# Kernel tuning notes

Hardware: AMD Instinct MI355X
Metric: run time of the kernel (lower is better)

The kernel has to match this reference:

```python
import jax, jax.numpy as jnp
import numpy as np

B, S, D, H, R = 2, 2048, 1024, 16, 64
DD = D // H  # head depth = 64
EPS = 1e-06


def setup_inputs() -> dict:
    key = jax.random.key(0)
    ks = jax.random.split(key, 12)
    sc = 1.0 / np.sqrt(D)
    inp = {
        'v': jax.random.normal(ks[0], (B, S, D), jnp.float32),
        'k': jax.random.normal(ks[1], (B, S, D), jnp.float32),
        'q': jax.random.normal(ks[2], (B, S, D), jnp.float32),
        'wq_w': jax.random.normal(ks[3], (D, D), jnp.float32) * sc,
        'wq_b': jnp.zeros((D,), jnp.float32),
        'wk_w': jax.random.normal(ks[4], (D, D), jnp.float32) * sc,
        'wk_b': jnp.zeros((D,), jnp.float32),
        'wv_w': jax.random.normal(ks[5], (D, D), jnp.float32) * sc,
        'wv_b': jnp.zeros((D,), jnp.float32),
        'wc_w': jax.random.normal(ks[6], (D, D), jnp.float32) * sc,
        'wc_b': jnp.zeros((D,), jnp.float32),
        # random-feature projection (orthogonal in original; gaussian suffices for a math-equivalent reference)
        'wg': jax.random.normal(ks[7], (H, DD, R), jnp.float32) * (1.0 / np.sqrt(DD)),
    }
    return inp


def _split_heads(x):
    # [B,S,D] -> [B,H,S,DD]
    return x.reshape(B, S, H, DD).transpose(0, 2, 1, 3)


def _combine_heads(x):
    # [B,H,S,DD] -> [B,S,D]
    return x.transpose(0, 2, 1, 3).reshape(B, S, D)


def _sm_approx(x, wg):
    # x: [B,H,S,DD], wg: [H,DD,R] -> phi(x): [B,H,S,R]
    rsqr_d = 1.0 / np.sqrt(DD)
    h_x = jnp.exp(-0.5 * jnp.sum(jnp.square(x), axis=-1, keepdims=True))
    phi_x = rsqr_d * jnp.exp(jnp.einsum('bhsd,hdr->bhsr', x, wg))
    return h_x * phi_x


def reference(v, k, q, wq_w, wq_b, wk_w, wk_b, wv_w, wv_b, wc_w, wc_b, wg):
    norm_d = float(DD) ** -0.25
    qh = _split_heads((q @ wq_w + wq_b) * norm_d)   # [B,H,S,DD]
    kh = _split_heads((k @ wk_w + wk_b) * norm_d)   # [B,H,S,DD]
    vh = _split_heads(v @ wv_w + wv_b)              # [B,H,S,DD]

    q_prime = _sm_approx(qh, wg)                    # [B,H,S,R]
    k_prime = _sm_approx(kh, wg)                    # [B,H,S,R]

    # per-position outer product k_prime (x) v : [B,H,S,R,DD]
    kv_prime = jnp.einsum('bhsr,bhsd->bhsrd', k_prime, vh)

    # causal prefix sums over sequence axis (k_prev/kv_prev = 0 case)
    k_prefix = jnp.cumsum(k_prime, axis=2)          # [B,H,S,R]
    kv_prefix = jnp.cumsum(kv_prime, axis=2)        # [B,H,S,R,DD]

    qk_prefix = jnp.sum(q_prime * k_prefix, axis=-1, keepdims=True)       # [B,H,S,1]
    attn_unnorm = jnp.einsum('bhsr,bhsrd->bhsd', q_prime, kv_prefix)      # [B,H,S,DD]
    attn = attn_unnorm / (EPS + qk_prefix)

    out = _combine_heads(attn) @ wc_w + wc_b        # [B,S,D]
    return (k_prefix, kv_prefix, out)
```

## Files before the change

kernel.cpp:

```cpp
#include <hip/hip_runtime.h>
#include <hip/hip_bf16.h>

#define BB 2
#define SS 2048
#define DD 1024
#define HH 16
#define RR 64
#define DH 64
#define BH (BB*HH)
#define MM (BB*SS)
#define CH 32
#define NCH (SS/CH)
#define CSROW (RR*DH + RR)

using short8 = __attribute__((ext_vector_type(8))) short;
using f32x4  = __attribute__((ext_vector_type(4))) float;

typedef const __attribute__((address_space(1))) unsigned int* gp_t;
typedef __attribute__((address_space(3))) unsigned int* lp_t;

__device__ __forceinline__ void gll16(const void* g, void* l) {
    __builtin_amdgcn_global_load_lds((gp_t)g, (lp_t)l, 16, 0, 0);
}

__device__ __forceinline__ unsigned short f2bf(float x) {
    __hip_bfloat16 h = __float2bfloat16(x);
    return *(unsigned short*)&h;
}

__global__ __launch_bounds__(256) void k_pre(
    const float* __restrict__ q, const float* __restrict__ k, const float* __restrict__ v,
    const float* __restrict__ bq, const float* __restrict__ bk, const float* __restrict__ bv,
    const float* __restrict__ wq, const float* __restrict__ wk,
    const float* __restrict__ wv, const float* __restrict__ wc,
    const float* __restrict__ wg,
    __hip_bfloat16* __restrict__ Xb, float* __restrict__ biasb,
    __hip_bfloat16* __restrict__ WT, __hip_bfloat16* __restrict__ wcT,
    short* __restrict__ wgbT)
{
    int bid = blockIdx.x;
    __shared__ float tile[64][65];
    if (bid < 12288) {
        int z = bid >> 12;
        int bx = bid & 4095;
        const float* src = (z == 0) ? q : (z == 1) ? k : v;
        size_t i = ((size_t)bx * 256 + threadIdx.x) * 4;
        float4 f = *(const float4*)(src + i);
        __hip_bfloat16* dst = Xb + (size_t)z * 4194304 + i;
        dst[0] = __float2bfloat16(f.x);
        dst[1] = __float2bfloat16(f.y);
        dst[2] = __float2bfloat16(f.z);
        dst[3] = __float2bfloat16(f.w);
        if (bx == 0) {
            const float* bb = (z == 0) ? bq : (z == 1) ? bk : bv;
            for (int t = threadIdx.x; t < 1024; t += 256)
                biasb[z * 1024 + t] = bb[t];
        }
    } else if (bid < 13312) {
        int sub = bid - 12288;
        int zz = sub >> 8;
        sub &= 255;
        const float* W = (zz == 0) ? wq : (zz == 1) ? wk : (zz == 2) ? wv : wc;
        __hip_bfloat16* T = (zz < 3) ? (WT + (size_t)zz * 1048576) : wcT;
        int k0 = (sub >> 4) * 64, n0 = (sub & 15) * 64;
        for (int i = threadIdx.x; i < 4096; i += 256) {
            int r = i >> 6, cc = i & 63;
            tile[r][cc] = W[(size_t)(k0 + r) * 1024 + n0 + cc];
        }
        __syncthreads();
        for (int i = threadIdx.x; i < 4096; i += 256) {
            int nl = i >> 6, kl = i & 63;
            T[(size_t)(n0 + nl) * 1024 + k0 + kl] = __float2bfloat16(tile[kl][nl]);
        }
    } else {
        int hx = bid - 13312;
        for (int i = threadIdx.x; i < 4096; i += 256)
            tile[i >> 6][i & 63] = wg[(size_t)hx * 4096 + i];
        __syncthreads();
        for (int i = threadIdx.x; i < 4096; i += 256) {
            int r = i >> 6, d = i & 63;
            wgbT[(size_t)hx * 4096 + r * 64 + d] = (short)f2bf(tile[d][r]);
        }
    }
}

__global__ __launch_bounds__(256) void gemm_bt(
    const __hip_bfloat16* __restrict__ X, const __hip_bfloat16* __restrict__ WT,
    const float* __restrict__ bias, float* __restrict__ Cout,
    const short* __restrict__ wgbT,
    float* __restrict__ qp_out, float* __restrict__ kp_out2,
    long zsX, long zsW, long zsB, long zsC, int mode)
{
    const int K = 1024, N = 1024;
    int z = blockIdx.z;
    const short* Xz = (const short*)(X + (size_t)z * zsX);
    const short* Wz = (const short*)(WT + (size_t)z * zsW);
    const float* bz = bias + (size_t)z * zsB;
    float* Cz = Cout + (size_t)z * zsC;

    int bid = blockIdx.y * gridDim.x + blockIdx.x;
    int nb_cnt = gridDim.x * gridDim.y;
    int cpx = nb_cnt >> 3;
    int swz = (bid & 7) * cpx + (bid >> 3);
    int nb = swz % gridDim.x;
    int mb = swz / gridDim.x;
    int m0 = mb * 128;
    int n0 = nb * 128;

    __shared__ short smem[18432];
    short* As = smem;
    short* Bs = smem + 4096;
    short* wgT = smem;
    short* xw  = smem + 9216;

    int tid = threadIdx.x;
    int lane = tid & 63;
    int w = tid >> 6;
    int wm = (w >> 1) * 64, wn = (w & 1) * 64;

    f32x4 acc[4][4] = {};

    int srow = tid >> 2;
    int scol = (tid & 3) * 8;
    const short* Ag = Xz + (size_t)(m0 + srow) * K + scol;
    const short* Bg = Wz + (size_t)(n0 + srow) * K + scol;
    short* lA0 = As + tid * 8;
    short* lA1 = As + 64 * 32 + tid * 8;
    short* lB0 = Bs + tid * 8;
    short* lB1 = Bs + 64 * 32 + tid * 8;

    int fr = lane & 15, kg = (lane >> 4) * 8;

    for (int kt = 0; kt < K / 32; ++kt) {
        __syncthreads();
        gll16(Ag + kt * 32, lA0);
        gll16(Ag + (size_t)64 * K + kt * 32, lA1);
        gll16(Bg + kt * 32, lB0);
        gll16(Bg + (size_t)64 * K + kt * 32, lB1);
        __syncthreads();

        short8 af[4], bf[4];
#pragma unroll
        for (int mi = 0; mi < 4; ++mi)
            af[mi] = *(const short8*)&As[(wm + mi * 16 + fr) * 32 + kg];
#pragma unroll
        for (int ni = 0; ni < 4; ++ni)
            bf[ni] = *(const short8*)&Bs[(wn + ni * 16 + fr) * 32 + kg];
#pragma unroll
        for (int mi = 0; mi < 4; ++mi)
#pragma unroll
            for (int ni = 0; ni < 4; ++ni)
                acc[mi][ni] = __builtin_amdgcn_mfma_f32_16x16x32_bf16(af[mi], bf[ni], acc[mi][ni], 0, 0, 0);
    }

    int g = lane >> 4, c4 = lane & 15;

    if (mode == 1 && z < 2) {
        const float nd = 0.35355339059327373f;
        float* O = (z == 0) ? qp_out : kp_out2;
        int h = nb * 2 + (w & 1);
        int b = m0 >> 11;
        float bias_n[4];
#pragma unroll
        for (int ni = 0; ni < 4; ++ni) bias_n[ni] = bz[n0 + wn + ni * 16 + c4];

        __syncthreads();
        {
            int row = tid >> 2, part = tid & 3;
#pragma unroll
            for (int hl = 0; hl < 2; ++hl) {
                const short* src = wgbT + ((size_t)(nb * 2 + hl)) * 4096 + row * 64 + part * 16;
                short8 v0 = *(const short8*)src;
                short8 v1 = *(const short8*)(src + 8);
                *(short8*)&wgT[hl * 4608 + row * 72 + part * 16] = v0;
                *(short8*)&wgT[hl * 4608 + row * 72 + part * 16 + 8] = v1;
            }
        }
        __syncthreads();

        short* xww = xw + w * 2304;
        const short* wgh = wgT + (w & 1) * 4608;

#pragma unroll
        for (int pass = 0; pass < 2; ++pass) {
            float nrm[2][4];
#pragma unroll
            for (int mi_l = 0; mi_l < 2; ++mi_l) {
                int mi = pass * 2 + mi_l;
                float part_n[4] = {0.f, 0.f, 0.f, 0.f};
#pragma unroll
                for (int ni = 0; ni < 4; ++ni)
#pragma unroll
                    for (int i = 0; i < 4; ++i) {
                        float xv = (acc[mi][ni][i] + bias_n[ni]) * nd;
                        part_n[i] += xv * xv;
                        xww[(mi_l * 16 + g * 4 + i) * 72 + ni * 16 + c4] = (short)f2bf(xv);
                    }
#pragma unroll
                for (int i = 0; i < 4; ++i) {
                    float t = part_n[i];
                    t += __shfl_xor(t, 1, 64);
                    t += __shfl_xor(t, 2, 64);
                    t += __shfl_xor(t, 4, 64);
                    t += __shfl_xor(t, 8, 64);
                    nrm[mi_l][i] = t;
                }
            }
            short8 afr[2][2], bfr[4][2];
#pragma unroll
            for (int mi_l = 0; mi_l < 2; ++mi_l)
#pragma unroll
                for (int kk = 0; kk < 2; ++kk)
                    afr[mi_l][kk] = *(const short8*)&xww[(mi_l * 16 + c4) * 72 + kk * 32 + g * 8];
#pragma unroll
            for (int ri = 0; ri < 4; ++ri)
#pragma unroll
                for (int kk = 0; kk < 2; ++kk)
                    bfr[ri][kk] = *(const short8*)&wgh[(ri * 16 + c4) * 72 + kk * 32 + g * 8];
            f32x4 p[2][4] = {};
#pragma unroll
            for (int mi_l = 0; mi_l < 2; ++mi_l)
#pragma unroll
                for (int ri = 0; ri < 4; ++ri)
#pragma unroll
                    for (int kk = 0; kk < 2; ++kk)
                        p[mi_l][ri] = __builtin_amdgcn_mfma_f32_16x16x32_bf16(afr[mi_l][kk], bfr[ri][kk], p[mi_l][ri], 0, 0, 0);
#pragma unroll
            for (int mi_l = 0; mi_l < 2; ++mi_l)
#pragma unroll
                for (int ri = 0; ri < 4; ++ri)
#pragma unroll
                    for (int i = 0; i < 4; ++i) {
                        int mi = pass * 2 + mi_l;
                        float val = 0.125f * __expf(p[mi_l][ri][i] - 0.5f * nrm[mi_l][i]);
                        int row = m0 + wm + mi * 16 + g * 4 + i;
                        int s = row & 2047;
                        O[((size_t)(b * 16 + h) * SS + s) * RR + ri * 16 + c4] = val;
                    }
        }
        return;
    }

    int rg = g * 4;
#pragma unroll
    for (int mi = 0; mi < 4; ++mi)
#pragma unroll
        for (int ni = 0; ni < 4; ++ni) {
            int gn = n0 + wn + ni * 16 + fr;
            float bval = bz[gn];
#pragma unroll
            for (int i = 0; i < 4; ++i) {
                int gm = m0 + wm + mi * 16 + rg + i;
                Cz[(size_t)gm * N + gn] = acc[mi][ni][i] + bval;
            }
        }
}

__global__ __launch_bounds__(64) void k_chunksum(
    const float* __restrict__ kprime, const float* __restrict__ vh,
    float* __restrict__ cs)
{
    int c = blockIdx.x;
    int bh = blockIdx.y;
    int b = bh >> 4, h = bh & 15;
    int lane = threadIdx.x;
    __shared__ float kp[CH][RR];
    __shared__ float vv[CH][RR];
    size_t rowbase = (size_t)bh * SS + c * CH;
    const float* vbase = vh + ((size_t)b * SS + c * CH) * DD + h * DH;
#pragma unroll
    for (int i = 0; i < 8; ++i) {
        int flat = i * 64 + lane;
        int row = flat >> 4, q4 = flat & 15;
        *(f32x4*)&kp[row][q4 * 4] = *(const f32x4*)&kprime[(rowbase + row) * RR + q4 * 4];
        *(f32x4*)&vv[row][q4 * 4] = *(const f32x4*)&vbase[(size_t)row * DD + q4 * 4];
    }
    __syncthreads();

    float st[RR];
#pragma unroll
    for (int r = 0; r < RR; ++r) st[r] = 0.f;
    float kpsum = 0.f;
    for (int s = 0; s < CH; ++s) {
        float vd = vv[s][lane];
        kpsum += kp[s][lane];
#pragma unroll
        for (int rq = 0; rq < RR / 4; ++rq) {
            f32x4 kq = *(const f32x4*)&kp[s][rq * 4];
            st[rq * 4 + 0] += kq[0] * vd;
            st[rq * 4 + 1] += kq[1] * vd;
            st[rq * 4 + 2] += kq[2] * vd;
            st[rq * 4 + 3] += kq[3] * vd;
        }
    }
    float* out = cs + (size_t)(bh * NCH + c) * CSROW;
#pragma unroll
    for (int r = 0; r < RR; ++r) out[r * 64 + lane] = st[r];
    out[4096 + lane] = kpsum;
}

__global__ __launch_bounds__(256) void k_scan(float* __restrict__ cs)
{
    int t = blockIdx.x * 256 + threadIdx.x;
    if (t >= BH * CSROW) return;
    int bh = t / CSROW;
    int e = t - bh * CSROW;
    float* p = cs + (size_t)bh * NCH * CSROW + e;
    float v[NCH];
#pragma unroll
    for (int c = 0; c < NCH; ++c) v[c] = p[(size_t)c * CSROW];
    float run = 0.f;
#pragma unroll
    for (int c = 0; c < NCH; ++c) {
        float x = v[c];
        p[(size_t)c * CSROW] = run;
        run += x;
    }
}

__global__ __launch_bounds__(64) void k_scanfinal(
    const float* __restrict__ kprime, const float* __restrict__ qprime,
    const float* __restrict__ vh, const float* __restrict__ cs,
    float* __restrict__ kp_out, float* __restrict__ kv_out,
    __hip_bfloat16* __restrict__ attnb)
{
    int c = blockIdx.x;
    int bh = blockIdx.y;
    int b = bh >> 4, h = bh & 15;
    int lane = threadIdx.x;
    int g = lane >> 4, c4 = lane & 15;
    __shared__ float kp[CH][RR];
    __shared__ float qp[CH][RR];
    __shared__ float vv[CH][RR];
    size_t rowbase = (size_t)bh * SS + c * CH;
    const float* vbase = vh + ((size_t)b * SS + c * CH) * DD + h * DH;
#pragma unroll
    for (int i = 0; i < 8; ++i) {
        int flat = i * 64 + lane;
        int row = flat >> 4, q4 = flat & 15;
        *(f32x4*)&kp[row][q4 * 4] = *(const f32x4*)&kprime[(rowbase + row) * RR + q4 * 4];
        *(f32x4*)&qp[row][q4 * 4] = *(const f32x4*)&qprime[(rowbase + row) * RR + q4 * 4];
        *(f32x4*)&vv[row][q4 * 4] = *(const f32x4*)&vbase[(size_t)row * DD + q4 * 4];
    }

    const float* off = cs + (size_t)(bh * NCH + c) * CSROW;
    f32x4 st[16];
#pragma unroll
    for (int j = 0; j < 16; ++j)
        st[j] = *(const f32x4*)&off[(4 * j + g) * 64 + 4 * c4];
    float kps = off[4096 + lane];
    __syncthreads();

    for (int s = 0; s < CH; ++s) {
        float kpl = kp[s][lane];
        kps += kpl;
        size_t srow = rowbase + s;
        kp_out[srow * RR + lane] = kps;

        float qksum = qp[s][lane] * kps;
#pragma unroll
        for (int m = 1; m < 64; m <<= 1) qksum += __shfl_xor(qksum, m, 64);

        f32x4 v4 = *(const f32x4*)&vv[s][4 * c4];
        f32x4 accp = {0.f, 0.f, 0.f, 0.f};
        float* kvp = kv_out + srow * (size_t)(RR * DH);
#pragma unroll
        for (int j = 0; j < 16; ++j) {
            float kpj = kp[s][4 * j + g];
            float qpj = qp[s][4 * j + g];
            st[j] += kpj * v4;
            __builtin_nontemporal_store(st[j], (f32x4*)(kvp + (4 * j + g) * 64 + 4 * c4));
            accp += qpj * st[j];
        }
#pragma unroll
        for (int e = 0; e < 4; ++e) {
            accp[e] += __shfl_xor(accp[e], 16, 64);
            accp[e] += __shfl_xor(accp[e], 32, 64);
        }
        float rs = 1.0f / (1e-6f + qksum);
        if (g == 0) {
            ushort4 pkt;
            pkt.x = f2bf(accp[0] * rs);
            pkt.y = f2bf(accp[1] * rs);
            pkt.z = f2bf(accp[2] * rs);
            pkt.w = f2bf(accp[3] * rs);
            *(ushort4*)((unsigned short*)attnb + ((size_t)b * SS + c * CH + s) * DD + h * DH + 4 * c4) = pkt;
        }
    }
}

extern "C" void kernel_launch(void* const* d_in, const int* in_sizes, int n_in,
                              void* d_out, int out_size, void* d_ws, size_t ws_size,
                              hipStream_t stream) {
    const float* v_in  = (const float*)d_in[0];
    const float* k_in  = (const float*)d_in[1];
    const float* q_in  = (const float*)d_in[2];
    const float* wq_w  = (const float*)d_in[3];
    const float* wq_b  = (const float*)d_in[4];
    const float* wk_w  = (const float*)d_in[5];
    const float* wk_b  = (const float*)d_in[6];
    const float* wv_w  = (const float*)d_in[7];
    const float* wv_b  = (const float*)d_in[8];
    const float* wc_w  = (const float*)d_in[9];
    const float* wc_b  = (const float*)d_in[10];
    const float* wg    = (const float*)d_in[11];

    char* ws = (char*)d_ws;
    __hip_bfloat16* Xb    = (__hip_bfloat16*)(ws + 0);
    __hip_bfloat16* WT    = (__hip_bfloat16*)(ws + 25165824);
    __hip_bfloat16* wcT   = (__hip_bfloat16*)(ws + 31457280);
    float* biasb          = (float*)(ws + 33554432);
    float* qhkv           = (float*)(ws + 33570816);
    float* qprime         = (float*)(ws + 83902464);
    float* kprime         = (float*)(ws + 100679680);
    float* cs             = (float*)(ws + 117456896);
    __hip_bfloat16* attnb = (__hip_bfloat16*)(ws + 151535616);
    short* wgbT           = (short*)(ws + 159924224);

    float* kp_out = (float*)d_out;
    float* kv_out = kp_out + 4194304;
    float* out_o  = kv_out + 268435456;
    float* vh     = qhkv + 2 * 4194304;

    k_pre<<<dim3(13328), 256, 0, stream>>>(q_in, k_in, v_in, wq_b, wk_b, wv_b,
                                           wq_w, wk_w, wv_w, wc_w, wg,
                                           Xb, biasb, WT, wcT, wgbT);
    gemm_bt<<<dim3(8, 32, 3), 256, 0, stream>>>(Xb, WT, biasb, qhkv, wgbT, qprime, kprime,
                                                4194304L, 1048576L, 1024L, 4194304L, 1);
    k_chunksum<<<dim3(NCH, BH), 64, 0, stream>>>(kprime, vh, cs);
    k_scan<<<dim3(520), 256, 0, stream>>>(cs);
    k_scanfinal<<<dim3(NCH, BH), 64, 0, stream>>>(kprime, qprime, vh, cs,
                                                  kp_out, kv_out, attnb);
    gemm_bt<<<dim3(8, 32, 1), 256, 0, stream>>>(attnb, wcT, wc_b, out_o, wgbT, qprime, kprime,
                                                0L, 0L, 0L, 0L, 0);
}
```

Baseline: 342.4 us.

## Store q'/k'/v intermediates as bf16 and deepen GEMM K-tile to 64

```diff
diff --git a/kernel.cpp b/kernel.cpp
--- a/kernel.cpp
+++ b/kernel.cpp
@@ -26,6 +26,10 @@
 __device__ __forceinline__ unsigned short f2bf(float x) {
     __hip_bfloat16 h = __float2bfloat16(x);
     return *(unsigned short*)&h;
+}
+
+__device__ __forceinline__ float bf2f(unsigned short u) {
+    return __uint_as_float(((unsigned int)u) << 16);
 }
 
 __global__ __launch_bounds__(256) void k_pre(
@@ -88,7 +92,7 @@
     const __hip_bfloat16* __restrict__ X, const __hip_bfloat16* __restrict__ WT,
     const float* __restrict__ bias, float* __restrict__ Cout,
     const short* __restrict__ wgbT,
-    float* __restrict__ qp_out, float* __restrict__ kp_out2,
+    unsigned short* __restrict__ qp_out, unsigned short* __restrict__ kp_out2,
     long zsX, long zsW, long zsB, long zsC, int mode)
 {
     const int K = 1024, N = 1024;
@@ -109,7 +113,7 @@
 
     __shared__ short smem[18432];
     short* As = smem;
-    short* Bs = smem + 4096;
+    short* Bs = smem + 8192;
     short* wgT = smem;
     short* xw  = smem + 9216;
 
@@ -124,40 +128,45 @@
     int scol = (tid & 3) * 8;
     const short* Ag = Xz + (size_t)(m0 + srow) * K + scol;
     const short* Bg = Wz + (size_t)(n0 + srow) * K + scol;
-    short* lA0 = As + tid * 8;
-    short* lA1 = As + 64 * 32 + tid * 8;
-    short* lB0 = Bs + tid * 8;
-    short* lB1 = Bs + 64 * 32 + tid * 8;
 
     int fr = lane & 15, kg = (lane >> 4) * 8;
 
-    for (int kt = 0; kt < K / 32; ++kt) {
-        __syncthreads();
-        gll16(Ag + kt * 32, lA0);
-        gll16(Ag + (size_t)64 * K + kt * 32, lA1);
-        gll16(Bg + kt * 32, lB0);
-        gll16(Bg + (size_t)64 * K + kt * 32, lB1);
-        __syncthreads();
-
-        short8 af[4], bf[4];
-#pragma unroll
-        for (int mi = 0; mi < 4; ++mi)
-            af[mi] = *(const short8*)&As[(wm + mi * 16 + fr) * 32 + kg];
-#pragma unroll
-        for (int ni = 0; ni < 4; ++ni)
-            bf[ni] = *(const short8*)&Bs[(wn + ni * 16 + fr) * 32 + kg];
-#pragma unroll
-        for (int mi = 0; mi < 4; ++mi)
+    for (int kt = 0; kt < K / 64; ++kt) {
+        const short* Ak = Ag + kt * 64;
+        const short* Bk = Bg + kt * 64;
+        __syncthreads();
+        gll16(Ak,                      As + tid * 8);
+        gll16(Ak + (size_t)64 * K,     As + 2048 + tid * 8);
+        gll16(Ak + 32,                 As + 4096 + tid * 8);
+        gll16(Ak + 32 + (size_t)64 * K, As + 6144 + tid * 8);
+        gll16(Bk,                      Bs + tid * 8);
+        gll16(Bk + (size_t)64 * K,     Bs + 2048 + tid * 8);
+        gll16(Bk + 32,                 Bs + 4096 + tid * 8);
+        gll16(Bk + 32 + (size_t)64 * K, Bs + 6144 + tid * 8);
+        __syncthreads();
+
+#pragma unroll
+        for (int kk = 0; kk < 2; ++kk) {
+            short8 af[4], bf[4];
+#pragma unroll
+            for (int mi = 0; mi < 4; ++mi)
+                af[mi] = *(const short8*)&As[kk * 4096 + (wm + mi * 16 + fr) * 32 + kg];
 #pragma unroll
             for (int ni = 0; ni < 4; ++ni)
-                acc[mi][ni] = __builtin_amdgcn_mfma_f32_16x16x32_bf16(af[mi], bf[ni], acc[mi][ni], 0, 0, 0);
+                bf[ni] = *(const short8*)&Bs[kk * 4096 + (wn + ni * 16 + fr) * 32 + kg];
+#pragma unroll
+            for (int mi = 0; mi < 4; ++mi)
+#pragma unroll
+                for (int ni = 0; ni < 4; ++ni)
+                    acc[mi][ni] = __builtin_amdgcn_mfma_f32_16x16x32_bf16(af[mi], bf[ni], acc[mi][ni], 0, 0, 0);
+        }
     }
 
     int g = lane >> 4, c4 = lane & 15;
 
     if (mode == 1 && z < 2) {
         const float nd = 0.35355339059327373f;
-        float* O = (z == 0) ? qp_out : kp_out2;
+        unsigned short* O = (z == 0) ? qp_out : kp_out2;
         int h = nb * 2 + (w & 1);
         int b = m0 >> 11;
         float bias_n[4];
@@ -235,13 +244,30 @@
                         float val = 0.125f * __expf(p[mi_l][ri][i] - 0.5f * nrm[mi_l][i]);
                         int row = m0 + wm + mi * 16 + g * 4 + i;
                         int s = row & 2047;
-                        O[((size_t)(b * 16 + h) * SS + s) * RR + ri * 16 + c4] = val;
+                        O[((size_t)(b * 16 + h) * SS + s) * RR + ri * 16 + c4] = f2bf(val);
                     }
         }
         return;
     }
 
     int rg = g * 4;
+    if (mode == 1) {
+        unsigned short* Cz16 = (unsigned short*)Cz;
+#pragma unroll
+        for (int mi = 0; mi < 4; ++mi)
+#pragma unroll
+            for (int ni = 0; ni < 4; ++ni) {
+                int gn = n0 + wn + ni * 16 + fr;
+                float bval = bz[gn];
+#pragma unroll
+                for (int i = 0; i < 4; ++i) {
+                    int gm = m0 + wm + mi * 16 + rg + i;
+                    Cz16[(size_t)gm * N + gn] = f2bf(acc[mi][ni][i] + bval);
+                }
+            }
+        return;
+    }
+
 #pragma unroll
     for (int mi = 0; mi < 4; ++mi)
 #pragma unroll
@@ -257,7 +283,7 @@
 }
 
 __global__ __launch_bounds__(64) void k_chunksum(
-    const float* __restrict__ kprime, const float* __restrict__ vh,
+    const unsigned short* __restrict__ kprime, const unsigned short* __restrict__ vh,
     float* __restrict__ cs)
 {
     int c = blockIdx.x;
@@ -267,13 +293,19 @@
     __shared__ float kp[CH][RR];
     __shared__ float vv[CH][RR];
     size_t rowbase = (size_t)bh * SS + c * CH;
-    const float* vbase = vh + ((size_t)b * SS + c * CH) * DD + h * DH;
-#pragma unroll
-    for (int i = 0; i < 8; ++i) {
+    const unsigned short* kpb = kprime + rowbase * RR;
+    const unsigned short* vb = vh + ((size_t)b * SS + c * CH) * DD + h * DH;
+#pragma unroll
+    for (int i = 0; i < 4; ++i) {
         int flat = i * 64 + lane;
-        int row = flat >> 4, q4 = flat & 15;
-        *(f32x4*)&kp[row][q4 * 4] = *(const f32x4*)&kprime[(rowbase + row) * RR + q4 * 4];
-        *(f32x4*)&vv[row][q4 * 4] = *(const f32x4*)&vbase[(size_t)row * DD + q4 * 4];
+        int row = flat >> 3, c8 = (flat & 7) * 8;
+        short8 k8 = *(const short8*)(kpb + (size_t)row * RR + c8);
+        short8 v8 = *(const short8*)(vb + (size_t)row * DD + c8);
+#pragma unroll
+        for (int e = 0; e < 8; ++e) {
+            kp[row][c8 + e] = bf2f((unsigned short)k8[e]);
+            vv[row][c8 + e] = bf2f((unsigned short)v8[e]);
+        }
     }
     __syncthreads();
 
@@ -319,8 +351,8 @@
 }
 
 __global__ __launch_bounds__(64) void k_scanfinal(
-    const float* __restrict__ kprime, const float* __restrict__ qprime,
-    const float* __restrict__ vh, const float* __restrict__ cs,
+    const unsigned short* __restrict__ kprime, const unsigned short* __restrict__ qprime,
+    const unsigned short* __restrict__ vh, const float* __restrict__ cs,
     float* __restrict__ kp_out, float* __restrict__ kv_out,
     __hip_bfloat16* __restrict__ attnb)
 {
@@ -333,14 +365,22 @@
     __shared__ float qp[CH][RR];
     __shared__ float vv[CH][RR];
     size_t rowbase = (size_t)bh * SS + c * CH;
-    const float* vbase = vh + ((size_t)b * SS + c * CH) * DD + h * DH;
-#pragma unroll
-    for (int i = 0; i < 8; ++i) {
+    const unsigned short* kpb = kprime + rowbase * RR;
+    const unsigned short* qpb = qprime + rowbase * RR;
+    const unsigned short* vb = vh + ((size_t)b * SS + c * CH) * DD + h * DH;
+#pragma unroll
+    for (int i = 0; i < 4; ++i) {
         int flat = i * 64 + lane;
-        int row = flat >> 4, q4 = flat & 15;
-        *(f32x4*)&kp[row][q4 * 4] = *(const f32x4*)&kprime[(rowbase + row) * RR + q4 * 4];
-        *(f32x4*)&qp[row][q4 * 4] = *(const f32x4*)&qprime[(rowbase + row) * RR + q4 * 4];
-        *(f32x4*)&vv[row][q4 * 4] = *(const f32x4*)&vbase[(size_t)row * DD + q4 * 4];
+        int row = flat >> 3, c8 = (flat & 7) * 8;
+        short8 k8 = *(const short8*)(kpb + (size_t)row * RR + c8);
+        short8 q8 = *(const short8*)(qpb + (size_t)row * RR + c8);
+        short8 v8 = *(const short8*)(vb + (size_t)row * DD + c8);
+#pragma unroll
+        for (int e = 0; e < 8; ++e) {
+            kp[row][c8 + e] = bf2f((unsigned short)k8[e]);
+            qp[row][c8 + e] = bf2f((unsigned short)q8[e]);
+            vv[row][c8 + e] = bf2f((unsigned short)v8[e]);
+        }
     }
 
     const float* off = cs + (size_t)(bh * NCH + c) * CSROW;
@@ -411,8 +451,8 @@
     __hip_bfloat16* wcT   = (__hip_bfloat16*)(ws + 31457280);
     float* biasb          = (float*)(ws + 33554432);
     float* qhkv           = (float*)(ws + 33570816);
-    float* qprime         = (float*)(ws + 83902464);
-    float* kprime         = (float*)(ws + 100679680);
+    unsigned short* qprime = (unsigned short*)(ws + 83902464);
+    unsigned short* kprime = (unsigned short*)(ws + 100679680);
     float* cs             = (float*)(ws + 117456896);
     __hip_bfloat16* attnb = (__hip_bfloat16*)(ws + 151535616);
     short* wgbT           = (short*)(ws + 159924224);
@@ -420,16 +460,16 @@
     float* kp_out = (float*)d_out;
     float* kv_out = kp_out + 4194304;
     float* out_o  = kv_out + 268435456;
-    float* vh     = qhkv + 2 * 4194304;
+    unsigned short* vh16 = (unsigned short*)(qhkv + 2 * 4194304);
 
     k_pre<<<dim3(13328), 256, 0, stream>>>(q_in, k_in, v_in, wq_b, wk_b, wv_b,
                                            wq_w, wk_w, wv_w, wc_w, wg,
                                            Xb, biasb, WT, wcT, wgbT);
     gemm_bt<<<dim3(8, 32, 3), 256, 0, stream>>>(Xb, WT, biasb, qhkv, wgbT, qprime, kprime,
                                                 4194304L, 1048576L, 1024L, 4194304L, 1);
-    k_chunksum<<<dim3(NCH, BH), 64, 0, stream>>>(kprime, vh, cs);
+    k_chunksum<<<dim3(NCH, BH), 64, 0, stream>>>(kprime, vh16, cs);
     k_scan<<<dim3(520), 256, 0, stream>>>(cs);
-    k_scanfinal<<<dim3(NCH, BH), 64, 0, stream>>>(kprime, qprime, vh, cs,
+    k_scanfinal<<<dim3(NCH, BH), 64, 0, stream>>>(kprime, qprime, vh16, cs,
                                                   kp_out, kv_out, attnb);
     gemm_bt<<<dim3(8, 32, 1), 256, 0, stream>>>(attnb, wcT, wc_b, out_o, wgbT, qprime, kprime,
                                                 0L, 0L, 0L, 0L, 0);
```

Result: faster. 330.3 us (-3.5%).
